# Performance work log

Hardware: AMD Instinct MI355X
Metric: run time of the kernel (lower is better)

Reference implementation:

```python
import jax, jax.numpy as jnp
import numpy as np

HEADS = 8
TOK = 4  # num_query_tokens
EPS = 1e-5


def _ln(x, w, b):
    mu = jnp.mean(x, -1, keepdims=True)
    v = jnp.var(x, -1, keepdims=True)
    return (x - mu) / jnp.sqrt(v + EPS) * w + b


def _inorm(x):
    # InstanceNorm3d(affine=False): normalize per (B,C) over spatial dims
    mu = jnp.mean(x, (2, 3, 4), keepdims=True)
    v = jnp.var(x, (2, 3, 4), keepdims=True)
    return (x - mu) / jnp.sqrt(v + EPS)


def _conv3(x, w, b):
    y = jax.lax.conv_general_dilated(x, w, (1, 1, 1), 'SAME',
                                     dimension_numbers=('NCDHW', 'OIDHW', 'NCDHW'))
    return y + b[None, :, None, None, None]


def setup_inputs() -> dict:
    key = jax.random.key(0)
    ks = jax.random.split(key, 8)
    B, C, D, H, W = 4, 320, 16, 32, 32
    CLI = 320
    QD = C * TOK  # 1280
    s = 0.02
    return {
        'img_feat': jax.random.normal(ks[0], (B, C, D, H, W), jnp.float32),
        'cli_feat': jax.random.normal(ks[1], (B, CLI), jnp.float32),
        'Wq': jax.random.normal(ks[2], (QD, CLI), jnp.float32) * s,
        'bq': jnp.zeros((QD,), jnp.float32),
        'lnq_w': jnp.ones((QD,), jnp.float32),
        'lnq_b': jnp.zeros((QD,), jnp.float32),
        'Wk': jax.random.normal(ks[3], (C, C), jnp.float32) * s,
        'bk': jnp.zeros((C,), jnp.float32),
        'Wv': jax.random.normal(ks[4], (C, C), jnp.float32) * s,
        'bv': jnp.zeros((C,), jnp.float32),
        'Wo': jax.random.normal(ks[5], (C, QD), jnp.float32) * s,
        'bo': jnp.zeros((C,), jnp.float32),
        'lno_w': jnp.ones((C,), jnp.float32),
        'lno_b': jnp.zeros((C,), jnp.float32),
        'Wf1': jax.random.normal(ks[6], (C, 2 * C, 3, 3, 3), jnp.float32) * s,
        'bf1': jnp.zeros((C,), jnp.float32),
        'Wf2': jax.random.normal(ks[7], (C, C, 3, 3, 3), jnp.float32) * s,
        'bf2': jnp.zeros((C,), jnp.float32),
    }


def reference(img_feat, cli_feat, Wq, bq, lnq_w, lnq_b, Wk, bk, Wv, bv,
              Wo, bo, lno_w, lno_b, Wf1, bf1, Wf2, bf2):
    B, C, D, H, W = img_feat.shape
    S = D * H * W
    hd = C // HEADS
    scale = hd ** -0.5
    # clinical features -> 4 query tokens per head: [B, heads, head_dim, TOK]
    q = _ln(cli_feat @ Wq.T + bq, lnq_w, lnq_b).reshape(B, HEADS, hd, TOK)
    # 1x1x1 convs == per-position linear over channels
    x = img_feat.reshape(B, C, S)
    k = (jnp.einsum('oc,bcs->bos', Wk, x) + bk[None, :, None]).reshape(B, HEADS, hd, S)
    v = (jnp.einsum('oc,bcs->bos', Wv, x) + bv[None, :, None]).reshape(B, HEADS, hd, S)
    # [B, heads, TOK, S] scores -> softmax over spatial
    attn = jax.nn.softmax(jnp.einsum('bhdt,bhds->bhts', q, k) * scale, axis=-1)
    # value @ attn^T -> [B, heads, head_dim, TOK], flatten like torch .view(B,-1)
    o = jnp.einsum('bhds,bhts->bhdt', v, attn).reshape(B, HEADS * hd * TOK)
    o = _ln(o @ Wo.T + bo, lno_w, lno_b)  # [B, C]
    bcast = jnp.broadcast_to(o[:, :, None, None, None], (B, C, D, H, W))
    fused = jnp.concatenate([img_feat, bcast], axis=1)  # [B, 2C, D, H, W]
    h = jax.nn.gelu(_inorm(_conv3(fused, Wf1, bf1)), approximate=False)
    h = _inorm(_conv3(h, Wf2, bf2))
    return h + img_feat
```

## Files before the change

kernel.cpp:

```cpp
#include <hip/hip_runtime.h>
#include <hip/hip_bf16.h>
#include <math.h>

typedef unsigned short u16;

#define DEV static __device__ __forceinline__

DEV float bfu(u16 u) { union { unsigned int i; float f; } v; v.i = ((unsigned int)u) << 16; return v.f; }
DEV u16 fbu(float f) { __hip_bfloat16 h = __float2bfloat16(f); return *reinterpret_cast<u16*>(&h); }

template <typename T> struct ModeOf;
template <> struct ModeOf<u16>   { static constexpr int v = 0; };
template <> struct ModeOf<float> { static constexpr int v = 1; };
template <typename T> DEV float ld(const void* p, size_t i);
template <> DEV float ld<u16>(const void* p, size_t i)   { return bfu(((const u16*)p)[i]); }
template <> DEV float ld<float>(const void* p, size_t i) { return ((const float*)p)[i]; }

template <typename T> DEV float4 ld4(const void* p, size_t i);
template <> DEV float4 ld4<u16>(const void* p, size_t i) {
    ushort4 v = *reinterpret_cast<const ushort4*>((const u16*)p + i);
    return make_float4(bfu(v.x), bfu(v.y), bfu(v.z), bfu(v.w));
}
template <> DEV float4 ld4<float>(const void* p, size_t i) {
    return *reinterpret_cast<const float4*>((const float*)p + i);
}

#define NB 4
#define NC 320
#define ND 16
#define NH 32
#define NW 32
#define NS 16384
#define NHD 40
#define NQD 1280
#define NR 32
#define NTOK 4
#define OUT_N (NB*NC*NS)
#define EPSV 1e-5f
#define SCALE 0.15811388300841898f

#define YKS 8
#define YCH (NS / YKS)

#define CSL 32
#define NSL 10
#define HALO_D 4
#define HALO_H 6
#define PIXW 34
#define NPIX (HALO_D*HALO_H*PIXW)
#define PACKN (27*10*20*64*8)

typedef __attribute__((ext_vector_type(8))) short bf16x8;
typedef __attribute__((ext_vector_type(4))) float f32x4;

DEV int swz4(int p) { return (p + (p >> 2)) & 3; }

DEV float blk_sum(float v, float* red) {
    __syncthreads();
#pragma unroll
    for (int o = 32; o > 0; o >>= 1) v += __shfl_down(v, o, 64);
    int wv = threadIdx.x >> 6, ln = threadIdx.x & 63;
    if (ln == 0) red[wv] = v;
    __syncthreads();
    return red[0] + red[1] + red[2] + red[3];
}
DEV float blk_max(float v, float* red) {
    __syncthreads();
#pragma unroll
    for (int o = 32; o > 0; o >>= 1) v = fmaxf(v, __shfl_down(v, o, 64));
    int wv = threadIdx.x >> 6, ln = threadIdx.x & 63;
    if (ln == 0) red[wv] = v;
    __syncthreads();
    return fmaxf(fmaxf(red[0], red[1]), fmaxf(red[2], red[3]));
}

__global__ void detect_kernel(const u16* __restrict__ lnqw, int* __restrict__ flag) {
    if (threadIdx.x == 0) flag[0] = (lnqw[0] == 0x3F80) ? 0 : 1;
}

template <typename T>
__global__ __launch_bounds__(256) void q_kernel(const int* __restrict__ flag,
        const void* __restrict__ cli, const void* __restrict__ Wq, const void* __restrict__ bq,
        const void* __restrict__ lnw, const void* __restrict__ lnb, float* __restrict__ qout) {
    if (*flag != ModeOf<T>::v) return;
    int b = blockIdx.x, tid = threadIdx.x;
    __shared__ float cl[NC];
    __shared__ float red[8];
    for (int i = tid; i < NC; i += 256) cl[i] = ld<T>(cli, b * NC + i);
    __syncthreads();
    float loc[5];
    float s1 = 0.f, s2 = 0.f;
#pragma unroll
    for (int k = 0; k < 5; ++k) {
        int j = tid + k * 256;
        float a = ld<T>(bq, j);
        size_t wr = (size_t)j * NC;
        for (int c = 0; c < NC; ++c) a += cl[c] * ld<T>(Wq, wr + c);
        loc[k] = a; s1 += a; s2 += a * a;
    }
    s1 = blk_sum(s1, red);
    s2 = blk_sum(s2, red);
    float mu = s1 / (float)NQD;
    float var = fmaxf(s2 / (float)NQD - mu * mu, 0.f);
    float rs = rsqrtf(var + EPSV);
#pragma unroll
    for (int k = 0; k < 5; ++k) {
        int j = tid + k * 256;
        qout[(size_t)b * NQD + j] = (loc[k] - mu) * rs * ld<T>(lnw, j) + ld<T>(lnb, j);
    }
}

template <typename T>
__global__ __launch_bounds__(256) void qw_kernel(const int* __restrict__ flag,
        const float* __restrict__ q, const void* __restrict__ Wk, const void* __restrict__ bk,
        float* __restrict__ qW, float* __restrict__ qb) {
    if (*flag != ModeOf<T>::v) return;
    int gid = blockIdx.x * 256 + threadIdx.x;
    if (gid < NB * NR * NC) {
        int c = gid % NC;
        int r = (gid / NC) % NR;
        int b = gid / (NC * NR);
        int h = r >> 2, t = r & 3;
        float a = 0.f;
        const float* qb_ = q + (size_t)b * NQD;
        for (int d = 0; d < NHD; ++d)
            a += qb_[(h * NHD + d) * NTOK + t] * ld<T>(Wk, (size_t)(h * NHD + d) * NC + c);
        qW[gid] = a;
    }
    if (gid < NB * NR) {
        int r = gid & 31, b = gid >> 5;
        int h = r >> 2, t = r & 3;
        float a = 0.f;
        const float* qb_ = q + (size_t)b * NQD;
        for (int d = 0; d < NHD; ++d)
            a += qb_[(h * NHD + d) * NTOK + t] * ld<T>(bk, h * NHD + d);
        qb[gid] = a;
    }
}

template <typename T>
__global__ __launch_bounds__(256) void scores_kernel(const int* __restrict__ flag,
        const void* __restrict__ img, const float* __restrict__ qW, const float* __restrict__ qb,
        float* __restrict__ attn) {
    if (*flag != ModeOf<T>::v) return;
    int b = blockIdx.y;
    int s = blockIdx.x * 256 + threadIdx.x;
    __shared__ __align__(16) float qWl[NR * NC];
    for (int i = threadIdx.x; i < NR * NC; i += 256) qWl[i] = qW[(size_t)b * NR * NC + i];
    __syncthreads();
    float acc[NR];
#pragma unroll
    for (int r = 0; r < NR; ++r) acc[r] = 0.f;
    size_t xb = (size_t)b * NC * NS + s;
    for (int c0 = 0; c0 < NC; c0 += 4) {
        float x0 = ld<T>(img, xb + ((size_t)(c0 + 0) << 14));
        float x1 = ld<T>(img, xb + ((size_t)(c0 + 1) << 14));
        float x2 = ld<T>(img, xb + ((size_t)(c0 + 2) << 14));
        float x3 = ld<T>(img, xb + ((size_t)(c0 + 3) << 14));
#pragma unroll
        for (int r = 0; r < NR; ++r) {
            const float4 qv = *reinterpret_cast<const float4*>(&qWl[r * NC + c0]);
            acc[r] += qv.x * x0 + qv.y * x1 + qv.z * x2 + qv.w * x3;
        }
    }
#pragma unroll
    for (int r = 0; r < NR; ++r)
        attn[((size_t)(b * NR + r) << 14) + s] = (acc[r] + qb[b * NR + r]) * SCALE;
}

__global__ __launch_bounds__(256) void softmax_kernel(float* __restrict__ attn) {
    int row = blockIdx.x;
    float* rp = attn + ((size_t)row << 14);
    __shared__ float red[8];
    float m = -1e30f;
    for (int s = threadIdx.x; s < NS; s += 256) m = fmaxf(m, rp[s]);
    m = blk_max(m, red);
    float sum = 0.f;
    for (int s = threadIdx.x; s < NS; s += 256) {
        float e = expf(rp[s] - m);
        rp[s] = e; sum += e;
    }
    sum = blk_sum(sum, red);
    float inv = 1.f / sum;
    for (int s = threadIdx.x; s < NS; s += 256) rp[s] *= inv;
}

template <typename T>
__global__ __launch_bounds__(256) void y_kernel(const int* __restrict__ flag,
        const float* __restrict__ attn, const void* __restrict__ img, float* __restrict__ yp) {
    if (*flag != ModeOf<T>::v) return;
    int row = blockIdx.x;
    int ks  = blockIdx.y;
    int b = row >> 5;
    int wv = threadIdx.x >> 6, ln = threadIdx.x & 63;
    const float* ar = attn + ((size_t)row << 14) + ks * YCH;
    size_t xb = (size_t)b * NC * NS + ks * YCH;
    float* yout = yp + ((size_t)ks * NB * NR + row) * NC;
    for (int c = wv; c < NC; c += 4) {
        size_t xr = xb + ((size_t)c << 14);
        float p = 0.f;
#pragma unroll
        for (int it = 0; it < YCH / 256; ++it) {
            int s = it * 256 + ln * 4;
            float4 x = ld4<T>(img, xr + s);
            const float4 a = *reinterpret_cast<const float4*>(ar + s);
            p += a.x * x.x + a.y * x.y + a.z * x.z + a.w * x.w;
        }
#pragma unroll
        for (int o = 32; o > 0; o >>= 1) p += __shfl_down(p, o, 64);
        if (ln == 0) yout[c] = p;
    }
}

__global__ __launch_bounds__(256) void yred_kernel(const float* __restrict__ yp, float* __restrict__ y) {
    int i = blockIdx.x * 256 + threadIdx.x;
    if (i >= NB * NR * NC) return;
    float s = 0.f;
#pragma unroll
    for (int k = 0; k < YKS; ++k) s += yp[(size_t)k * NB * NR * NC + i];
    y[i] = s;
}

template <typename T>
__global__ __launch_bounds__(256) void o_kernel(const int* __restrict__ flag,
        const float* __restrict__ y, const void* __restrict__ Wv, const void* __restrict__ bv,
        const void* __restrict__ Wo, const void* __restrict__ bo,
        const void* __restrict__ lnw, const void* __restrict__ lnb, float* __restrict__ o2) {
    if (*flag != ModeOf<T>::v) return;
    int b = blockIdx.x, tid = threadIdx.x;
    __shared__ float yl[NR * NC];
    __shared__ float ol[NQD];
    __shared__ float red[8];
    for (int i = tid; i < NR * NC; i += 256) yl[i] = y[(size_t)b * NR * NC + i];
    __syncthreads();
#pragma unroll
    for (int k = 0; k < 5; ++k) {
        int i = tid + k * 256;
        int h = i / 160, rem = i - h * 160;
        int d = rem >> 2, t = rem & 3;
        int wr = h * NHD + d, r = h * NTOK + t;
        float a = ld<T>(bv, wr);
        size_t wvr = (size_t)wr * NC;
        const float* yr = yl + r * NC;
        for (int c = 0; c < NC; ++c) a += ld<T>(Wv, wvr + c) * yr[c];
        ol[i] = a;
    }
    __syncthreads();
    for (int j = tid; j < NC; j += 256) {
        float a = ld<T>(bo, j);
        size_t wor = (size_t)j * NQD;
        for (int i = 0; i < NQD; ++i) a += ld<T>(Wo, wor + i) * ol[i];
        yl[j] = a;
    }
    __syncthreads();
    float s1 = 0.f, s2 = 0.f;
    for (int j = tid; j < NC; j += 256) { float v = yl[j]; s1 += v; s2 += v * v; }
    s1 = blk_sum(s1, red);
    s2 = blk_sum(s2, red);
    float mu = s1 / (float)NC;
    float var = fmaxf(s2 / (float)NC - mu * mu, 0.f);
    float rs = rsqrtf(var + EPSV);
    for (int j = tid; j < NC; j += 256)
        o2[(size_t)b * NC + j] = (yl[j] - mu) * rs * ld<T>(lnw, j) + ld<T>(lnb, j);
}

template <typename T>
__global__ __launch_bounds__(256) void p_kernel(const int* __restrict__ flag,
        const float* __restrict__ o2, const void* __restrict__ Wf1, float* __restrict__ P) {
    if (*flag != ModeOf<T>::v) return;
    int o = blockIdx.x, b = blockIdx.y;
    int tid = threadIdx.x, wv = tid >> 6, ln = tid & 63;
    __shared__ float red[4 * 27];
    __shared__ float taps[27];
    float acc[27];
#pragma unroll
    for (int k = 0; k < 27; ++k) acc[k] = 0.f;
    for (int c = tid; c < NC; c += 256) {
        float oc = o2[(size_t)b * NC + c];
        size_t wp = ((size_t)o * 640 + 320 + c) * 27;
#pragma unroll
        for (int k = 0; k < 27; ++k) acc[k] += oc * ld<T>(Wf1, wp + k);
    }
#pragma unroll
    for (int k = 0; k < 27; ++k) {
        float v = acc[k];
#pragma unroll
        for (int off = 32; off > 0; off >>= 1) v += __shfl_down(v, off, 64);
        if (ln == 0) red[wv * 27 + k] = v;
    }
    __syncthreads();
    if (tid < 27) taps[tid] = red[tid] + red[27 + tid] + red[54 + tid] + red[81 + tid];
    __syncthreads();
    if (tid < 27) {
        int pd = tid / 9, ph = (tid / 3) % 3, pw = tid % 3;
        float s = 0.f;
        for (int kd = 0; kd < 3; ++kd) {
            if ((pd == 0 && kd == 0) || (pd == 2 && kd == 2)) continue;
            for (int kh = 0; kh < 3; ++kh) {
                if ((ph == 0 && kh == 0) || (ph == 2 && kh == 2)) continue;
                for (int kw = 0; kw < 3; ++kw) {
                    if ((pw == 0 && kw == 0) || (pw == 2 && kw == 2)) continue;
                    s += taps[kd * 9 + kh * 3 + kw];
                }
            }
        }
        P[(size_t)(b * NC + o) * 27 + tid] = s;
    }
}

template <typename T>
__global__ __launch_bounds__(256) void imgt_kernel(const int* __restrict__ flag,
        const void* __restrict__ img, u16* __restrict__ outT) {
    if (*flag != ModeOf<T>::v) return;
    int b = blockIdx.z, c0 = blockIdx.y << 5, s0 = blockIdx.x << 5;
    int r = threadIdx.x >> 3, c4 = (threadIdx.x & 7) << 2;
    __shared__ float tile[32][33];
#pragma unroll
    for (int j = 0; j < 4; ++j)
        tile[r][c4 + j] = ld<T>(img, ((size_t)(b * NC + c0 + r) << 14) + s0 + c4 + j);
    __syncthreads();
    u16* op = outT + ((size_t)b * NS + s0 + r) * NC + c0 + c4;
#pragma unroll
    for (int j = 0; j < 4; ++j) op[j] = fbu(tile[c4 + j][r]);
}

template <typename TW>
__global__ __launch_bounds__(256) void pack_kernel(const int* __restrict__ flag,
        const void* __restrict__ wgt, const void* __restrict__ bias,
        u16* __restrict__ wpack, float* __restrict__ biasf, int wic) {
    if (*flag != ModeOf<TW>::v) return;
    int gid = blockIdx.x * 256 + threadIdx.x;
    if (gid < NC) biasf[gid] = ld<TW>(bias, gid);
    int lane = gid & 63;
    int rest = gid >> 6;
    int obg = rest % 20;  rest /= 20;
    int t = rest % 27;    int cs = rest / 27;
    int o  = (obg << 4) + (lane & 15);
    int c0 = (cs << 5) + ((lane >> 4) << 3);
    u16* dst = wpack + (size_t)gid * 8;
#pragma unroll
    for (int j = 0; j < 8; ++j)
        dst[j] = fbu(ld<TW>(wgt, ((size_t)o * wic + c0 + j) * 27 + t));
}

__global__ __launch_bounds__(256, 3) void convmm_kernel(
        const u16* __restrict__ inT, const u16* __restrict__ wpack,
        const float* __restrict__ biasf, const float* __restrict__ Pp,
        u16* __restrict__ out) {
    int d0 = (blockIdx.x >> 3) << 1;
    int h0 = (blockIdx.x & 7) << 2;
    int ob = blockIdx.y;
    int b  = blockIdx.z;
    int tid = threadIdx.x;
    int wv = tid >> 6, ln = tid & 63;
    int col = ln & 15, g = ln >> 4;

    __shared__ __align__(16) u16 lin[NPIX * CSL];

    {
        float4 z = {0.f, 0.f, 0.f, 0.f};
        float4* lp = reinterpret_cast<float4*>(lin);
        for (int i = tid; i < NPIX * CSL / 8; i += 256) lp[i] = z;
    }
    __syncthreads();

    f32x4 acc[4][4];
#pragma unroll
    for (int mi = 0; mi < 4; ++mi)
#pragma unroll
        for (int ni = 0; ni < 4; ++ni) acc[mi][ni] = (f32x4){0.f, 0.f, 0.f, 0.f};

    int pix0[4];
#pragma unroll
    for (int ni = 0; ni < 4; ++ni) {
        int nb = (wv << 2) + ni;
        int r2 = nb >> 1;
        int ddo = r2 >> 2, hho = r2 & 3;
        pix0[ni] = (ddo * HALO_H + hho) * PIXW + ((nb & 1) << 4) + col;
    }

    size_t inb = (size_t)b * NS * NC;

    for (int cs = 0; cs < NSL; ++cs) {
        for (int k = wv; k < 48; k += 4) {
            int hf = k & 1, rr = k >> 1;
            int dd = rr / HALO_H, hh = rr - dd * HALO_H;
            int dg = d0 + dd - 1, hg = h0 + hh - 1;
            if ((unsigned)dg < ND && (unsigned)hg < NH) {
                int pixbase = (dd * HALO_H + hh) * PIXW + 1 + (hf << 4);
                int p = pixbase + (ln >> 2);
                int wpos = (hf << 4) + (ln >> 2);
                int cg = (ln & 3) ^ swz4(p);
                const u16* src = inT + inb + ((size_t)(dg << 10) + (hg << 5) + wpos) * NC
                                 + (cs << 5) + (cg << 3);
                __builtin_amdgcn_global_load_lds(
                    (const __attribute__((address_space(1))) unsigned int*)src,
                    (__attribute__((address_space(3))) unsigned int*)(lin + pixbase * CSL),
                    16, 0, 0);
            }
        }
        __syncthreads();

        const u16* wp = wpack + (size_t)cs * 27 * 20 * 512;
#pragma unroll
        for (int t = 0; t < 27; ++t) {
            const int kd = t / 9, kh = (t / 3) % 3, kw = t % 3;
            bf16x8 af[4];
#pragma unroll
            for (int mi = 0; mi < 4; ++mi)
                af[mi] = *reinterpret_cast<const bf16x8*>(
                    wp + ((size_t)(t * 20 + (ob << 2) + mi) << 9) + (ln << 3));
            bf16x8 bfr[4];
#pragma unroll
            for (int ni = 0; ni < 4; ++ni) {
                int p = pix0[ni] + (kd * HALO_H + kh) * PIXW + kw;
                bfr[ni] = *reinterpret_cast<const bf16x8*>(
                    lin + p * CSL + ((g ^ swz4(p)) << 3));
            }
#pragma unroll
            for (int mi = 0; mi < 4; ++mi)
#pragma unroll
                for (int ni = 0; ni < 4; ++ni)
                    acc[mi][ni] = __builtin_amdgcn_mfma_f32_16x16x32_bf16(
                        af[mi], bfr[ni], acc[mi][ni], 0, 0, 0);
        }
        __syncthreads();
    }

#pragma unroll
    for (int ni = 0; ni < 4; ++ni) {
        int nb = (wv << 2) + ni;
        int r2 = nb >> 1;
        int d = d0 + (r2 >> 2);
        int h = h0 + (r2 & 3);
        int w = ((nb & 1) << 4) + col;
        int pd = (d == 0) ? 0 : ((d == ND - 1) ? 2 : 1);
        int ph = (h == 0) ? 0 : ((h == NH - 1) ? 2 : 1);
        int pw = (w == 0) ? 0 : ((w == NW - 1) ? 2 : 1);
        size_t sidx = ((size_t)d << 10) + (h << 5) + w;
#pragma unroll
        for (int mi = 0; mi < 4; ++mi) {
#pragma unroll
            for (int r = 0; r < 4; ++r) {
                int o = (ob << 6) + (mi << 4) + (g << 2) + r;
                float v = acc[mi][ni][r] + biasf[o];
                if (Pp) v += Pp[(size_t)(b * NC + o) * 27 + pd * 9 + ph * 3 + pw];
                out[((size_t)(b * NC + o) << 14) + sidx] = fbu(v);
            }
        }
    }
}

__global__ __launch_bounds__(256) void stats_kernel(const u16* __restrict__ raw, float* __restrict__ mean,
                                                    float* __restrict__ rstd) {
    int bo = blockIdx.x;
    const u16* base = raw + ((size_t)bo << 14);
    __shared__ float red[8];
    float s1 = 0.f, s2 = 0.f;
    for (int s = threadIdx.x; s < NS; s += 256) { float v = bfu(base[s]); s1 += v; s2 += v * v; }
    s1 = blk_sum(s1, red);
    s2 = blk_sum(s2, red);
    if (threadIdx.x == 0) {
        float mu = s1 / (float)NS;
        float var = fmaxf(s2 / (float)NS - mu * mu, 0.f);
        mean[bo] = mu;
        rstd[bo] = rsqrtf(var + EPSV);
    }
}

__global__ __launch_bounds__(256) void norm1t_kernel(const u16* __restrict__ raw,
        const float* __restrict__ mean, const float* __restrict__ rstd, u16* __restrict__ h1t) {
    int b = blockIdx.z, c0 = blockIdx.y << 5, s0 = blockIdx.x << 5;
    int r = threadIdx.x >> 3, c4 = (threadIdx.x & 7) << 2;
    __shared__ float tile[32][33];
    int bo = b * NC + c0 + r;
    float mu = mean[bo], rs = rstd[bo];
    const u16* rp = raw + ((size_t)bo << 14) + s0 + c4;
#pragma unroll
    for (int j = 0; j < 4; ++j) {
        float xn = (bfu(rp[j]) - mu) * rs;
        tile[r][c4 + j] = 0.5f * xn * (1.f + erff(xn * 0.70710678118654752f));
    }
    __syncthreads();
    u16* op = h1t + ((size_t)b * NS + s0 + r) * NC + c0 + c4;
#pragma unroll
    for (int j = 0; j < 4; ++j) op[j] = fbu(tile[c4 + j][r]);
}

template <typename T>
__global__ __launch_bounds__(256) void final_kernel(const int* __restrict__ flag,
        const u16* __restrict__ raw, const float* __restrict__ mean, const float* __restrict__ rstd,
        const void* __restrict__ img, void* __restrict__ outp) {
    if (*flag != ModeOf<T>::v) return;
    int idx = blockIdx.x * 256 + threadIdx.x;
    if (idx >= OUT_N) return;
    int bo = idx >> 14;
    float xn = (bfu(raw[idx]) - mean[bo]) * rstd[bo];
    float r = xn + ld<T>(img, idx);
    if (ModeOf<T>::v == 0) ((u16*)outp)[idx] = fbu(r);
    else                   ((float*)outp)[idx] = r;
}

extern "C" void kernel_launch(void* const* d_in, const int* in_sizes, int n_in,
                              void* d_out, int out_size, void* d_ws, size_t ws_size,
                              hipStream_t stream) {
    const void* IMG  = d_in[0];
    const void* CLI  = d_in[1];
    const void* WQ   = d_in[2];
    const void* BQ   = d_in[3];
    const void* LNQW = d_in[4];
    const void* LNQB = d_in[5];
    const void* WK   = d_in[6];
    const void* BK   = d_in[7];
    const void* WV   = d_in[8];
    const void* BV   = d_in[9];
    const void* WO   = d_in[10];
    const void* BO   = d_in[11];
    const void* LNOW = d_in[12];
    const void* LNOB = d_in[13];
    const void* WF1  = d_in[14];
    const void* BF1  = d_in[15];
    const void* WF2  = d_in[16];
    const void* BF2  = d_in[17];

    char* ws = (char*)d_ws;
    size_t off = 0;
    auto alloc = [&](size_t bytes) { void* p = ws + off; off += (bytes + 255) & ~(size_t)255; return p; };
    int*   FLAG  = (int*)  alloc(256);
    u16*   RAW   = (u16*)  alloc((size_t)OUT_N * 2);
    float* Qf    = (float*)alloc((size_t)NB * NQD * 4);
    float* QW    = (float*)alloc((size_t)NB * NR * NC * 4);
    float* QB    = (float*)alloc((size_t)NB * NR * 4);
    float* Yb    = (float*)alloc((size_t)NB * NR * NC * 4);
    float* O2    = (float*)alloc((size_t)NB * NC * 4);
    float* PB    = (float*)alloc((size_t)NB * NC * 27 * 4);
    float* MEAN  = (float*)alloc((size_t)NB * NC * 4);
    float* RSTD  = (float*)alloc((size_t)NB * NC * 4);
    u16*   WPACK = (u16*)  alloc((size_t)PACKN * 2);
    float* BIASF = (float*)alloc((size_t)NC * 4);
    float* ATTN  = (float*)d_out;
    float* YP    = (float*)RAW;
    u16*   IMGT  = (u16*)d_out;
    u16*   H1    = (u16*)d_out;
    (void)ws_size; (void)n_in; (void)in_sizes; (void)out_size;

    detect_kernel<<<1, 64, 0, stream>>>((const u16*)LNQW, FLAG);

    q_kernel<u16>  <<<NB, 256, 0, stream>>>(FLAG, CLI, WQ, BQ, LNQW, LNQB, Qf);
    q_kernel<float><<<NB, 256, 0, stream>>>(FLAG, CLI, WQ, BQ, LNQW, LNQB, Qf);

    int qwg = (NB * NR * NC + 255) / 256;
    qw_kernel<u16>  <<<qwg, 256, 0, stream>>>(FLAG, Qf, WK, BK, QW, QB);
    qw_kernel<float><<<qwg, 256, 0, stream>>>(FLAG, Qf, WK, BK, QW, QB);

    scores_kernel<u16>  <<<dim3(64, NB), 256, 0, stream>>>(FLAG, IMG, QW, QB, ATTN);
    scores_kernel<float><<<dim3(64, NB), 256, 0, stream>>>(FLAG, IMG, QW, QB, ATTN);

    softmax_kernel<<<NB * NR, 256, 0, stream>>>(ATTN);

    y_kernel<u16>  <<<dim3(NB * NR, YKS), 256, 0, stream>>>(FLAG, ATTN, IMG, YP);
    y_kernel<float><<<dim3(NB * NR, YKS), 256, 0, stream>>>(FLAG, ATTN, IMG, YP);

    yred_kernel<<<(NB * NR * NC + 255) / 256, 256, 0, stream>>>(YP, Yb);

    imgt_kernel<u16>  <<<dim3(512, 10, NB), 256, 0, stream>>>(FLAG, IMG, IMGT);
    imgt_kernel<float><<<dim3(512, 10, NB), 256, 0, stream>>>(FLAG, IMG, IMGT);

    o_kernel<u16>  <<<NB, 256, 0, stream>>>(FLAG, Yb, WV, BV, WO, BO, LNOW, LNOB, O2);
    o_kernel<float><<<NB, 256, 0, stream>>>(FLAG, Yb, WV, BV, WO, BO, LNOW, LNOB, O2);

    p_kernel<u16>  <<<dim3(NC, NB), 256, 0, stream>>>(FLAG, O2, WF1, PB);
    p_kernel<float><<<dim3(NC, NB), 256, 0, stream>>>(FLAG, O2, WF1, PB);

    int pkg = (PACKN / 8 + 255) / 256;
    pack_kernel<u16>  <<<pkg, 256, 0, stream>>>(FLAG, WF1, BF1, WPACK, BIASF, 640);
    pack_kernel<float><<<pkg, 256, 0, stream>>>(FLAG, WF1, BF1, WPACK, BIASF, 640);

    convmm_kernel<<<dim3(64, 5, NB), 256, 0, stream>>>(IMGT, WPACK, BIASF, PB, RAW);

    stats_kernel<<<NB * NC, 256, 0, stream>>>(RAW, MEAN, RSTD);
    norm1t_kernel<<<dim3(512, 10, NB), 256, 0, stream>>>(RAW, MEAN, RSTD, H1);

    pack_kernel<u16>  <<<pkg, 256, 0, stream>>>(FLAG, WF2, BF2, WPACK, BIASF, 320);
    pack_kernel<float><<<pkg, 256, 0, stream>>>(FLAG, WF2, BF2, WPACK, BIASF, 320);

    convmm_kernel<<<dim3(64, 5, NB), 256, 0, stream>>>(H1, WPACK, BIASF, nullptr, RAW);

    stats_kernel<<<NB * NC, 256, 0, stream>>>(RAW, MEAN, RSTD);

    final_kernel<u16>  <<<(OUT_N + 255) / 256, 256, 0, stream>>>(FLAG, RAW, MEAN, RSTD, IMG, d_out);
    final_kernel<float><<<(OUT_N + 255) / 256, 256, 0, stream>>>(FLAG, RAW, MEAN, RSTD, IMG, d_out);
}
```

Measured before the change: 2.132 ms.

## Double-buffer conv fragment loads and remap blocks across XCDs

```diff
diff --git a/kernel.cpp b/kernel.cpp
--- a/kernel.cpp
+++ b/kernel.cpp
@@ -347,10 +347,13 @@
         const u16* __restrict__ inT, const u16* __restrict__ wpack,
         const float* __restrict__ biasf, const float* __restrict__ Pp,
         u16* __restrict__ out) {
-    int d0 = (blockIdx.x >> 3) << 1;
-    int h0 = (blockIdx.x & 7) << 2;
-    int ob = blockIdx.y;
-    int b  = blockIdx.z;
+    int id = blockIdx.x;
+    int nid = (id & 7) * 160 + (id >> 3);
+    int sp = nid % 64;
+    int ob = (nid / 64) % 5;
+    int b  = nid / 320;
+    int d0 = (sp >> 3) << 1;
+    int h0 = (sp & 7) << 2;
     int tid = threadIdx.x;
     int wv = tid >> 6, ln = tid & 63;
     int col = ln & 15, g = ln >> 4;
@@ -380,6 +383,19 @@
     }
 
     size_t inb = (size_t)b * NS * NC;
+
+#define FETCH(T, AF, BF) {                                                        \
+    const int kd_ = (T) / 9, kh_ = ((T) / 3) % 3, kw_ = (T) % 3;                  \
+    _Pragma("unroll")                                                             \
+    for (int mi = 0; mi < 4; ++mi)                                                \
+        AF[mi] = *reinterpret_cast<const bf16x8*>(                                \
+            wp + ((size_t)((T) * 20 + (ob << 2) + mi) << 9) + (ln << 3));         \
+    _Pragma("unroll")                                                             \
+    for (int ni = 0; ni < 4; ++ni) {                                              \
+        int p_ = pix0[ni] + (kd_ * HALO_H + kh_) * PIXW + kw_;                    \
+        BF[ni] = *reinterpret_cast<const bf16x8*>(                                \
+            lin + p_ * CSL + ((g ^ swz4(p_)) << 3));                              \
+    } }
 
     for (int cs = 0; cs < NSL; ++cs) {
         for (int k = wv; k < 48; k += 4) {
@@ -402,30 +418,24 @@
         __syncthreads();
 
         const u16* wp = wpack + (size_t)cs * 27 * 20 * 512;
+        bf16x8 afA[4], bfrA[4];
+        FETCH(0, afA, bfrA);
 #pragma unroll
         for (int t = 0; t < 27; ++t) {
-            const int kd = t / 9, kh = (t / 3) % 3, kw = t % 3;
-            bf16x8 af[4];
-#pragma unroll
-            for (int mi = 0; mi < 4; ++mi)
-                af[mi] = *reinterpret_cast<const bf16x8*>(
-                    wp + ((size_t)(t * 20 + (ob << 2) + mi) << 9) + (ln << 3));
-            bf16x8 bfr[4];
-#pragma unroll
-            for (int ni = 0; ni < 4; ++ni) {
-                int p = pix0[ni] + (kd * HALO_H + kh) * PIXW + kw;
-                bfr[ni] = *reinterpret_cast<const bf16x8*>(
-                    lin + p * CSL + ((g ^ swz4(p)) << 3));
-            }
+            bf16x8 afB[4], bfrB[4];
+            if (t < 26) FETCH(t + 1, afB, bfrB);
 #pragma unroll
             for (int mi = 0; mi < 4; ++mi)
 #pragma unroll
                 for (int ni = 0; ni < 4; ++ni)
                     acc[mi][ni] = __builtin_amdgcn_mfma_f32_16x16x32_bf16(
-                        af[mi], bfr[ni], acc[mi][ni], 0, 0, 0);
+                        afA[mi], bfrA[ni], acc[mi][ni], 0, 0, 0);
+#pragma unroll
+            for (int i = 0; i < 4; ++i) { afA[i] = afB[i]; bfrA[i] = bfrB[i]; }
         }
         __syncthreads();
     }
+#undef FETCH
 
 #pragma unroll
     for (int ni = 0; ni < 4; ++ni) {
@@ -576,7 +586,7 @@
     pack_kernel<u16>  <<<pkg, 256, 0, stream>>>(FLAG, WF1, BF1, WPACK, BIASF, 640);
     pack_kernel<float><<<pkg, 256, 0, stream>>>(FLAG, WF1, BF1, WPACK, BIASF, 640);
 
-    convmm_kernel<<<dim3(64, 5, NB), 256, 0, stream>>>(IMGT, WPACK, BIASF, PB, RAW);
+    convmm_kernel<<<1280, 256, 0, stream>>>(IMGT, WPACK, BIASF, PB, RAW);
 
     stats_kernel<<<NB * NC, 256, 0, stream>>>(RAW, MEAN, RSTD);
     norm1t_kernel<<<dim3(512, 10, NB), 256, 0, stream>>>(RAW, MEAN, RSTD, H1);
@@ -584,7 +594,7 @@
     pack_kernel<u16>  <<<pkg, 256, 0, stream>>>(FLAG, WF2, BF2, WPACK, BIASF, 320);
     pack_kernel<float><<<pkg, 256, 0, stream>>>(FLAG, WF2, BF2, WPACK, BIASF, 320);
 
-    convmm_kernel<<<dim3(64, 5, NB), 256, 0, stream>>>(H1, WPACK, BIASF, nullptr, RAW);
+    convmm_kernel<<<1280, 256, 0, stream>>>(H1, WPACK, BIASF, nullptr, RAW);
 
     stats_kernel<<<NB * NC, 256, 0, stream>>>(RAW, MEAN, RSTD);
 
```

Result: slower. 2.296 ms (+7.7%).
